# Kernel tuning notes

Hardware: AMD Instinct MI355X
Metric: run time of the kernel (lower is better)

## Reference

```python
import jax, jax.numpy as jnp
import numpy as np

B, F, DIM = 32, 2048, 1024
H, DH, Q, DEPTH, MULT = 16, 64, 64, 6, 2
INNER = H * DH  # 1024
EPS = 1e-5


def _ln(x, g, b):
    m = jnp.mean(x, axis=-1, keepdims=True)
    v = jnp.mean((x - m) ** 2, axis=-1, keepdims=True)
    return (x - m) / jnp.sqrt(v + EPS) * g + b


def setup_inputs() -> dict:
    key = jax.random.key(0)
    ks = iter(jax.random.split(key, 32))
    def rn(shape, s=0.02):
        return jax.random.normal(next(ks), shape, dtype=jnp.float32) * s
    inp = {
        "features": jax.random.normal(next(ks), (B, F, DIM), dtype=jnp.float32),
        "mask": jax.random.randint(next(ks), (B, F), 0, 2),
        "latents": jax.random.normal(next(ks), (Q, INNER), dtype=jnp.float32),
        "W_down": rn((DIM, INNER)),
        "nin_g": jnp.ones((DIM,)), "nin_b": jnp.zeros((DIM,)),
        "lf_g": jnp.ones((DEPTH, INNER)), "lf_b": jnp.zeros((DEPTH, INNER)),
        "ll_g": jnp.ones((DEPTH, INNER)), "ll_b": jnp.zeros((DEPTH, INNER)),
        "Wq": rn((DEPTH, INNER, INNER)),
        "Wk": rn((DEPTH, INNER, INNER)),
        "Wv": rn((DEPTH, INNER, INNER)),
        "ffln_g": jnp.ones((DEPTH, INNER)), "ffln_b": jnp.zeros((DEPTH, INNER)),
        "ff_w1": rn((DEPTH, INNER, MULT * INNER)),
        "ff_w2": rn((DEPTH, MULT * INNER, INNER)),
        "nout_g": jnp.ones((INNER,)), "nout_b": jnp.zeros((INNER,)),
    }
    return inp


def reference(features, mask, latents, W_down, nin_g, nin_b, lf_g, lf_b, ll_g, ll_b,
              Wq, Wk, Wv, ffln_g, ffln_b, ff_w1, ff_w2, nout_g, nout_b):
    scale = DH ** (-0.5)
    # input norm + projection down to inner_dim
    f = _ln(features, nin_g, nin_b) @ W_down            # (B, F, INNER)
    x = jnp.broadcast_to(latents, (B, Q, INNER))        # (B, Q, INNER)
    keep = (mask != 0)[:, None, None, :]                # (B, 1, 1, F)
    for i in range(DEPTH):
        xf = _ln(f, lf_g[i], lf_b[i])
        xl = _ln(x, ll_g[i], ll_b[i])
        q = (xl @ Wq[i]).reshape(B, Q, H, DH).transpose(0, 2, 1, 3) * scale  # bhqd
        k = (xf @ Wk[i]).reshape(B, F, H, DH).transpose(0, 2, 1, 3)          # bhfd
        v = (xf @ Wv[i]).reshape(B, F, H, DH).transpose(0, 2, 1, 3)          # bhfd
        sim = jnp.einsum('bhqd,bhfd->bhqf', q, k)
        sim = sim - jax.lax.stop_gradient(jnp.max(sim, axis=-1, keepdims=True))
        sim = jnp.where(keep, sim, -jnp.inf)
        alphas = jax.nn.softmax(sim, axis=-1)
        alphas = jnp.nan_to_num(alphas, nan=0.0)        # fully-masked rows -> 0
        out = jnp.einsum('bhqf,bhfd->bqhd', alphas, v).reshape(B, Q, INNER)
        # feed-forward: LN -> Linear -> ReLU -> Linear
        h = jax.nn.relu(_ln(out, ffln_g[i], ffln_b[i]) @ ff_w1[i]) @ ff_w2[i]
        x = x + h
    return _ln(x, nout_g, nout_b)
```

## Files before the change

### kernel.cpp

```cpp
#include <hip/hip_runtime.h>
#include <stdint.h>


#define DEV static __device__ __forceinline__

typedef __attribute__((ext_vector_type(8))) short short8;
typedef __attribute__((ext_vector_type(4))) float f32x4;
typedef __attribute__((ext_vector_type(4))) int int4v;
typedef __attribute__((ext_vector_type(4))) unsigned short ushort4v;
typedef unsigned short ushort_t;

DEV float bf2f(ushort_t u){ union{uint32_t i; float f;} x; x.i = ((uint32_t)u)<<16; return x.f; }
DEV ushort_t f2bf(float f){
  union{float f; uint32_t i;} x; x.f = f;
  uint32_t r = x.i + 0x7fffu + ((x.i>>16)&1u);
  return (ushort_t)(r>>16);
}

#define GLOAD16(gp, lp) __builtin_amdgcn_global_load_lds( \
    (const __attribute__((address_space(1))) uint32_t*)(gp), \
    (__attribute__((address_space(3))) uint32_t*)(lp), 16, 0, 0)

#define VMCNT(n) asm volatile("s_waitcnt vmcnt(" #n ")" ::: "memory")
#define CFENCE   asm volatile("" ::: "memory")
#define MFMA16(a,b,c) __builtin_amdgcn_mfma_f32_16x16x32_bf16(a,b,c,0,0,0)
#define MFMAI8(a,b,c) __builtin_amdgcn_mfma_i32_16x16x64_i8(a,b,c,0,0,0)

template<int NXB>
DEV void xcd_remapN(int g, int total, int& x, int& y){
  int xcd = g & 7;
  int k = g >> 3;
  int rows_per_xcd = (total / NXB) >> 3;
  y = xcd * rows_per_xcd + (k / NXB);
  x = k % NXB;
}

DEV void wreduce2(float& a, float& b){
  #pragma unroll
  for (int d = 32; d; d >>= 1){ a += __shfl_xor(a, d); b += __shfl_xor(b, d); }
}

__global__ __launch_bounds__(256) void k_compact(const int* __restrict__ mask,
                                                 int* __restrict__ idx, int* __restrict__ cnt){
  int b = blockIdx.x, t = threadIdx.x;
  const int* mb = mask + b*2048;
  int keep[8]; int c = 0;
  #pragma unroll
  for (int u = 0; u < 8; ++u){ keep[u] = (mb[t*8+u] != 0); c += keep[u]; }
  __shared__ int s[256];
  s[t] = c; __syncthreads();
  for (int off = 1; off < 256; off <<= 1){
    int v = (t >= off) ? s[t-off] : 0;
    __syncthreads();
    s[t] += v;
    __syncthreads();
  }
  int pos = s[t] - c;
  #pragma unroll
  for (int u = 0; u < 8; ++u) if (keep[u]) idx[b*2048 + pos++] = t*8 + u;
  if (t == 255) cnt[b] = s[255];
}

__global__ __launch_bounds__(256) void k_gather_norm(const float* __restrict__ feat,
        const int* __restrict__ idx, const int* __restrict__ cnt, ushort_t* __restrict__ outp){
  int w = threadIdx.x >> 6, l = threadIdx.x & 63;
  int row = blockIdx.x*4 + w;
  int b = row >> 11, j = row & 2047;
  if (j >= cnt[b]) return;
  int src = idx[b*2048 + j];
  const float* rp = feat + ((size_t)(b*2048 + src))*1024;
  float4 v[4]; float s = 0.f, q = 0.f;
  #pragma unroll
  for (int i = 0; i < 4; ++i){
    v[i] = *(const float4*)(rp + i*256 + l*4);
    s += v[i].x+v[i].y+v[i].z+v[i].w;
    q += v[i].x*v[i].x+v[i].y*v[i].y+v[i].z*v[i].z+v[i].w*v[i].w;
  }
  wreduce2(s, q);
  float mean = s * (1.f/1024.f);
  float rstd = rsqrtf(q*(1.f/1024.f) - mean*mean + 1e-5f);
  ushort_t* op = outp + (size_t)row*1024;
  #pragma unroll
  for (int i = 0; i < 4; ++i){
    ushort4v o;
    o.x = f2bf((v[i].x-mean)*rstd); o.y = f2bf((v[i].y-mean)*rstd);
    o.z = f2bf((v[i].z-mean)*rstd); o.w = f2bf((v[i].w-mean)*rstd);
    *(ushort4v*)(op + i*256 + l*4) = o;
  }
}

__global__ __launch_bounds__(256) void k_rownorm_i8(const ushort_t* __restrict__ in,
        int8_t* __restrict__ outp, float* __restrict__ sca, const int* __restrict__ cnt){
  int w = threadIdx.x >> 6, l = threadIdx.x & 63;
  int row = blockIdx.x*4 + w;
  if (cnt){ int b = row >> 11; if ((row & 2047) >= cnt[b]) return; }
  const ushort_t* rp = in + (size_t)row*1024 + l*16;
  float f[16]; float s = 0.f, q = 0.f;
  #pragma unroll
  for (int i = 0; i < 4; ++i){
    ushort4v u = *(const ushort4v*)(rp + i*4);
    f[i*4+0] = bf2f(u.x); f[i*4+1] = bf2f(u.y);
    f[i*4+2] = bf2f(u.z); f[i*4+3] = bf2f(u.w);
  }
  #pragma unroll
  for (int jj = 0; jj < 16; ++jj){ s += f[jj]; q += f[jj]*f[jj]; }
  wreduce2(s, q);
  float mean = s * (1.f/1024.f);
  float rstd = rsqrtf(q*(1.f/1024.f) - mean*mean + 1e-5f);
  float amax = 0.f;
  #pragma unroll
  for (int jj = 0; jj < 16; ++jj) amax = fmaxf(amax, fabsf(f[jj]-mean));
  #pragma unroll
  for (int d = 32; d; d >>= 1) amax = fmaxf(amax, __shfl_xor(amax, d));
  amax *= rstd;
  float inv = (amax > 0.f) ? 127.f/amax : 0.f;
  if (l == 0) sca[row] = amax * (1.f/127.f);
  uint32_t wds[4];
  #pragma unroll
  for (int i = 0; i < 4; ++i){
    uint32_t wd = 0;
    #pragma unroll
    for (int c = 0; c < 4; ++c){
      int qv = (int)rintf((f[i*4+c]-mean)*rstd*inv);
      wd |= ((uint32_t)(uint8_t)(int8_t)qv) << (c*8);
    }
    wds[i] = wd;
  }
  int4v pk; pk[0]=(int)wds[0]; pk[1]=(int)wds[1]; pk[2]=(int)wds[2]; pk[3]=(int)wds[3];
  *(int4v*)(outp + (size_t)row*1024 + l*16) = pk;
}

__global__ __launch_bounds__(256) void k_rownorm_f32_i8(const float* __restrict__ in,
        int8_t* __restrict__ outp, float* __restrict__ sca){
  int w = threadIdx.x >> 6, l = threadIdx.x & 63;
  int row = blockIdx.x*4 + w;
  const float* rp = in + (size_t)row*1024 + l*16;
  float f[16]; float s = 0.f, q = 0.f;
  #pragma unroll
  for (int i = 0; i < 4; ++i){
    float4 v = *(const float4*)(rp + i*4);
    f[i*4+0] = v.x; f[i*4+1] = v.y; f[i*4+2] = v.z; f[i*4+3] = v.w;
  }
  #pragma unroll
  for (int jj = 0; jj < 16; ++jj){ s += f[jj]; q += f[jj]*f[jj]; }
  wreduce2(s, q);
  float mean = s * (1.f/1024.f);
  float rstd = rsqrtf(q*(1.f/1024.f) - mean*mean + 1e-5f);
  float amax = 0.f;
  #pragma unroll
  for (int jj = 0; jj < 16; ++jj) amax = fmaxf(amax, fabsf(f[jj]-mean));
  #pragma unroll
  for (int d = 32; d; d >>= 1) amax = fmaxf(amax, __shfl_xor(amax, d));
  amax *= rstd;
  float inv = (amax > 0.f) ? 127.f/amax : 0.f;
  if (l == 0) sca[row] = amax * (1.f/127.f);
  uint32_t wds[4];
  #pragma unroll
  for (int i = 0; i < 4; ++i){
    uint32_t wd = 0;
    #pragma unroll
    for (int c = 0; c < 4; ++c){
      int qv = (int)rintf((f[i*4+c]-mean)*rstd*inv);
      wd |= ((uint32_t)(uint8_t)(int8_t)qv) << (c*8);
    }
    wds[i] = wd;
  }
  int4v pk; pk[0]=(int)wds[0]; pk[1]=(int)wds[1]; pk[2]=(int)wds[2]; pk[3]=(int)wds[3];
  *(int4v*)(outp + (size_t)row*1024 + l*16) = pk;
}

template<int PER>
__global__ __launch_bounds__(256) void k_quant_rows(const ushort_t* __restrict__ in,
        int8_t* __restrict__ outp, float* __restrict__ sca){
  const int K = PER*64;
  int w = threadIdx.x >> 6, l = threadIdx.x & 63;
  int row = blockIdx.x*4 + w;
  const ushort_t* rp = in + (size_t)row*K + l*PER;
  float f[PER];
  #pragma unroll
  for (int i = 0; i < PER/4; ++i){
    ushort4v u = *(const ushort4v*)(rp + i*4);
    f[i*4+0] = bf2f(u.x); f[i*4+1] = bf2f(u.y);
    f[i*4+2] = bf2f(u.z); f[i*4+3] = bf2f(u.w);
  }
  float amax = 0.f;
  #pragma unroll
  for (int jj = 0; jj < PER; ++jj) amax = fmaxf(amax, fabsf(f[jj]));
  #pragma unroll
  for (int d = 32; d; d >>= 1) amax = fmaxf(amax, __shfl_xor(amax, d));
  float inv = (amax > 0.f) ? 127.f/amax : 0.f;
  if (l == 0) sca[row] = amax * (1.f/127.f);
  #pragma unroll
  for (int vq = 0; vq < PER/16; ++vq){
    int4v pk;
    #pragma unroll
    for (int i = 0; i < 4; ++i){
      uint32_t wd = 0;
      #pragma unroll
      for (int c = 0; c < 4; ++c){
        int qv = (int)rintf(f[vq*16 + i*4 + c]*inv);
        wd |= ((uint32_t)(uint8_t)(int8_t)qv) << (c*8);
      }
      pk[i] = (int)wd;
    }
    *(int4v*)(outp + (size_t)row*K + l*PER + vq*16) = pk;
  }
}

__global__ __launch_bounds__(256) void k_final_ln(const float* __restrict__ x,
        const float* __restrict__ g, const float* __restrict__ bb, float* __restrict__ outp){
  int w = threadIdx.x >> 6, l = threadIdx.x & 63;
  int row = blockIdx.x*4 + w;
  const float* rp = x + (size_t)row*1024;
  float4 v[4]; float s = 0.f, q = 0.f;
  #pragma unroll
  for (int i = 0; i < 4; ++i){
    v[i] = *(const float4*)(rp + i*256 + l*4);
    s += v[i].x+v[i].y+v[i].z+v[i].w;
    q += v[i].x*v[i].x+v[i].y*v[i].y+v[i].z*v[i].z+v[i].w*v[i].w;
  }
  wreduce2(s, q);
  float mean = s * (1.f/1024.f);
  float rstd = rsqrtf(q*(1.f/1024.f) - mean*mean + 1e-5f);
  float* op = outp + (size_t)row*1024;
  #pragma unroll
  for (int i = 0; i < 4; ++i){
    float4 gg = *(const float4*)(g + i*256 + l*4);
    float4 bv = *(const float4*)(bb + i*256 + l*4);
    float4 o;
    o.x = (v[i].x-mean)*rstd*gg.x + bv.x; o.y = (v[i].y-mean)*rstd*gg.y + bv.y;
    o.z = (v[i].z-mean)*rstd*gg.z + bv.z; o.w = (v[i].w-mean)*rstd*gg.w + bv.w;
    *(float4*)(op + i*256 + l*4) = o;
  }
}

__global__ __launch_bounds__(256) void k_init_x(const float* __restrict__ lat, float* __restrict__ x){
  int v = blockIdx.x*256 + threadIdx.x;
  int row = v >> 8, cv = v & 255;
  ((float4*)x)[v] = ((const float4*)lat)[(row & 63)*256 + cv];
}

DEV void foldT_body(const float* __restrict__ W, const float* __restrict__ g,
                    float scale, ushort_t* __restrict__ Wt, int K, int N,
                    int n0, int k0){
  __shared__ float Ts[64][65];
  int t = threadIdx.x;
  #pragma unroll
  for (int i = 0; i < 4; ++i){
    int flat = i*1024 + t*4; int r = flat >> 6, c = flat & 63;
    float4 v = *(const float4*)(W + (size_t)(k0+r)*N + n0 + c);
    float gg = (g ? g[k0+r] : 1.f) * scale;
    Ts[r][c] = v.x*gg; Ts[r][c+1] = v.y*gg; Ts[r][c+2] = v.z*gg; Ts[r][c+3] = v.w*gg;
  }
  __syncthreads();
  #pragma unroll
  for (int i = 0; i < 4; ++i){
    int flat = i*1024 + t*4; int rn = flat >> 6, ck = flat & 63;
    ushort4v o;
    o.x = f2bf(Ts[ck][rn]);   o.y = f2bf(Ts[ck+1][rn]);
    o.z = f2bf(Ts[ck+2][rn]); o.w = f2bf(Ts[ck+3][rn]);
    *(ushort4v*)(Wt + (size_t)(n0+rn)*K + k0 + ck) = o;
  }
}

struct FDesc { const float* W; const float* g; ushort_t* dst; float scale; int K; int N; };
#define MAXFD 32
struct FoldTArgs { int cnt; FDesc d[MAXFD]; };

__global__ __launch_bounds__(256) void k_foldT_all(FoldTArgs a){
  const FDesc d = a.d[blockIdx.y];
  int nxb = d.N >> 6;
  int n0 = (blockIdx.x % nxb) * 64;
  int k0 = (blockIdx.x / nxb) * 64;
  if (k0 >= d.K) return;
  foldT_body(d.W, d.g, d.scale, d.dst, d.K, d.N, n0, k0);
}

DEV void foldBias_body(const float* __restrict__ W, const float* __restrict__ bvec,
                       float scale, float* __restrict__ bias, int K, int N, int o0){
  int t = threadIdx.x;
  int ol = t & 31, kc = t >> 5;
  int o = o0 + ol;
  int chunk = K >> 3;
  int c0 = kc*chunk, c1 = c0 + chunk;
  float s0 = 0, s1 = 0, s2 = 0, s3 = 0;
  for (int c = c0; c < c1; c += 4){
    s0 += bvec[c+0]*W[(size_t)(c+0)*N + o];
    s1 += bvec[c+1]*W[(size_t)(c+1)*N + o];
    s2 += bvec[c+2]*W[(size_t)(c+2)*N + o];
    s3 += bvec[c+3]*W[(size_t)(c+3)*N + o];
  }
  __shared__ float red[8][32];
  red[kc][ol] = (s0+s1)+(s2+s3);
  __syncthreads();
  if (kc == 0){
    float tot = 0;
    #pragma unroll
    for (int jj = 0; jj < 8; ++jj) tot += red[jj][ol];
    bias[o] = tot * scale;
  }
}

struct BDesc { const float* W; const float* b; float* dst; float scale; int K; int N; };
#define MAXBD 25
struct BiasArgs { int cnt; BDesc d[MAXBD]; };

__global__ __launch_bounds__(256) void k_foldBias_all(BiasArgs a){
  const BDesc d = a.d[blockIdx.y];
  int o0 = blockIdx.x * 32;
  if (o0 >= d.N) return;
  foldBias_body(d.W, d.b, d.scale, d.dst, d.K, d.N, o0);
}

template<int OUTMODE, int BN>
__global__ __launch_bounds__(256, 4) void k_gemm_sm(const int8_t* __restrict__ A,
        const int8_t* __restrict__ Bt, const float* __restrict__ sAr,
        const float* __restrict__ sBr, const float* __restrict__ bias,
        void* __restrict__ Cp, int M, int N, int Kb){
  constexpr int BM = 64;
  constexpr int NIF = BN/32;
  const int n0 = blockIdx.x * BN;
  const int m0 = blockIdx.y * BM;
  __shared__ __align__(16) char sA[2][BM*64];
  __shared__ __align__(16) char sB[2][BN*64];
  const int tid = threadIdx.x;
  const int wave = tid >> 6, lane = tid & 63;
  const int lo = lane & 15, hi = lane >> 4;
  const int wr = wave >> 1, wc = wave & 1;

  auto stage = [&](int buf, int k0){
    {
      int r = tid >> 2;
      int c = (tid & 3) ^ (r & 3);
      const int8_t* gp = A + (size_t)(m0 + r)*Kb + k0 + c*16;
      GLOAD16(gp, &sA[buf][0] + tid*16);
    }
    #pragma unroll
    for (int p = 0; p < BN/64; ++p){
      int r = p*64 + (tid >> 2);
      int c = (tid & 3) ^ (r & 3);
      const int8_t* gp = Bt + (size_t)(n0 + r)*Kb + k0 + c*16;
      GLOAD16(gp, &sB[buf][0] + p*4096 + tid*16);
    }
  };

  int4v acc[2][NIF] = {};
  stage(0, 0);
  const int nk = Kb >> 6;
  for (int ks = 0; ks < nk; ++ks){
    __syncthreads();
    if (ks + 1 < nk) stage((ks+1)&1, (ks+1) << 6);
    const int buf = ks & 1;
    int4v af[2], bfr[NIF];
    #pragma unroll
    for (int mi = 0; mi < 2; ++mi){
      int row = wr*(BM/2) + mi*16 + lo;
      af[mi] = *(const int4v*)(&sA[buf][row*64 + ((hi ^ (row & 3))*16)]);
    }
    #pragma unroll
    for (int ni = 0; ni < NIF; ++ni){
      int row = wc*(BN/2) + ni*16 + lo;
      bfr[ni] = *(const int4v*)(&sB[buf][row*64 + ((hi ^ (row & 3))*16)]);
    }
    #pragma unroll
    for (int mi = 0; mi < 2; ++mi)
      #pragma unroll
      for (int ni = 0; ni < NIF; ++ni)
        acc[mi][ni] = MFMAI8(af[mi], bfr[ni], acc[mi][ni]);
  }
  #pragma unroll
  for (int ni = 0; ni < NIF; ++ni){
    int col = n0 + wc*(BN/2) + ni*16 + lo;
    float bv = bias ? bias[col] : 0.f;
    float sb = sBr[col];
    #pragma unroll
    for (int mi = 0; mi < 2; ++mi){
      int rbase = m0 + wr*(BM/2) + mi*16 + hi*4;
      #pragma unroll
      for (int rr = 0; rr < 4; ++rr){
        int row = rbase + rr;
        float v = (float)acc[mi][ni][rr] * (sAr[row]*sb) + bv;
        size_t off = (size_t)row*N + col;
        if (OUTMODE == 0)      ((ushort_t*)Cp)[off] = f2bf(v);
        else if (OUTMODE == 1) ((ushort_t*)Cp)[off] = f2bf(fmaxf(v, 0.f));
        else                   ((float*)Cp)[off] += v;
      }
    }
  }
}

template<bool SKIP, int NXB>
__global__ __launch_bounds__(512, 2) void k_gemm256p8(const ushort_t* __restrict__ A,
        const ushort_t* __restrict__ Bt, const float* __restrict__ bias,
        ushort_t* __restrict__ Cp, int M, int N, int K, const int* __restrict__ cnt){
  int bx, by;
  xcd_remapN<NXB>(blockIdx.x, gridDim.x, bx, by);
  const int n0 = bx * 256;
  const int m0 = by * 256;
  if (SKIP){ int b = m0 >> 11; if ((m0 & 2047) >= cnt[b]) return; }
  __shared__ __align__(16) ushort_t sA[2][256*64];
  __shared__ __align__(16) ushort_t sB[2][256*64];
  const int tid = threadIdx.x;
  const int wave = tid >> 6, lane = tid & 63;
  const int lo = lane & 15, hi = lane >> 4;
  const int wm = wave >> 2, wn = wave & 3;
  const int srow = lane >> 3;
  const int schunk = (lane & 7) ^ srow;
  auto stageHalf = [&](ushort_t* dst, const ushort_t* __restrict__ G, int grow0,
                       int half, int k0){
    #pragma unroll
    for (int p = 0; p < 2; ++p){
      int rbase = half*128 + p*64 + wave*8;
      const ushort_t* gp = G + (size_t)(grow0 + rbase + srow)*K + k0 + schunk*8;
      char* lp = (char*)dst + (size_t)rbase*128;
      GLOAD16(gp, lp);
    }
  };
  auto ldsA = [&](int buf, int row, int kk)->short8{
    int ch = ((kk<<2) + hi) ^ (row & 7);
    return *(const short8*)((const char*)sA + (size_t)buf*32768 + (size_t)row*128 + ch*16);
  };
  auto ldsB = [&](int buf, int row, int kk)->short8{
    int ch = ((kk<<2) + hi) ^ (row & 7);
    return *(const short8*)((const char*)sB + (size_t)buf*32768 + (size_t)row*128 + ch*16);
  };
  f32x4 acc[8][4] = {};

  short8 af[4][2], bg[2][2];
#define LOADA(BUF, AH) \
    _Pragma("unroll") for (int mi_ = 0; mi_ < 4; ++mi_) \
      _Pragma("unroll") for (int kk_ = 0; kk_ < 2; ++kk_) \
        af[mi_][kk_] = ldsA(BUF, (AH)*128 + wm*64 + mi_*16 + lo, kk_);
#define LOADB(BUF, BH) \
    _Pragma("unroll") for (int nj_ = 0; nj_ < 2; ++nj_) \
      _Pragma("unroll") for (int kk_ = 0; kk_ < 2; ++kk_) \
        bg[nj_][kk_] = ldsB(BUF, (BH)*128 + wn*32 + nj_*16 + lo, kk_);
#define MMQ(AH, BH) \
    __builtin_amdgcn_s_barrier(); CFENCE; \
    __builtin_amdgcn_s_setprio(1); \
    _Pragma("unroll") for (int mi_ = 0; mi_ < 4; ++mi_) \
      _Pragma("unroll") for (int nj_ = 0; nj_ < 2; ++nj_) \
        _Pragma("unroll") for (int kk_ = 0; kk_ < 2; ++kk_) \
          acc[(AH)*4+mi_][(BH)*2+nj_] = \
            MFMA16(af[mi_][kk_], bg[nj_][kk_], acc[(AH)*4+mi_][(BH)*2+nj_]); \
    __builtin_amdgcn_s_setprio(0); CFENCE; \
    __builtin_amdgcn_s_barrier(); CFENCE;

  stageHalf(&sA[0][0], A,  m0, 0, 0);
  stageHalf(&sB[0][0], Bt, n0, 0, 0);
  stageHalf(&sA[0][0], A,  m0, 1, 0);
  stageHalf(&sB[0][0], Bt, n0, 1, 0);
  stageHalf(&sA[1][0], A,  m0, 0, 64);
  stageHalf(&sB[1][0], Bt, n0, 1, 64);
  VMCNT(4);
  __builtin_amdgcn_s_barrier();
  CFENCE;

  const int NI = K >> 7;
  for (int i = 0; i < NI; ++i){
    const int kt = i << 7;
    const bool lastI = (i == NI-1);
    LOADA(0,0) LOADB(0,0)
    stageHalf(&sA[1][0], A,  m0, 1, kt+64);
    MMQ(0,0)
    LOADB(0,1)
    stageHalf(&sB[1][0], Bt, n0, 0, kt+64);
    MMQ(0,1)
    LOADA(0,1)
    if (!lastI) stageHalf(&sA[0][0], A,  m0, 0, kt+128);
    MMQ(1,1)
    LOADB(0,0)
    if (!lastI) stageHalf(&sB[0][0], Bt, n0, 1, kt+128);
    if (lastI){ VMCNT(0); } else { VMCNT(4); }
    MMQ(1,0)
    LOADA(1,0) LOADB(1,0)
    if (!lastI) stageHalf(&sA[0][0], A,  m0, 1, kt+128);
    MMQ(0,0)
    LOADB(1,1)
    if (!lastI) stageHalf(&sB[0][0], Bt, n0, 0, kt+128);
    MMQ(0,1)
    LOADA(1,1)
    if (!lastI) stageHalf(&sA[1][0], A,  m0, 0, kt+192);
    MMQ(1,1)
    LOADB(1,0)
    if (!lastI){ stageHalf(&sB[1][0], Bt, n0, 1, kt+192); VMCNT(4); }
    MMQ(1,0)
  }
#undef LOADA
#undef LOADB
#undef MMQ

  #pragma unroll
  for (int b2 = 0; b2 < 2; ++b2)
    #pragma unroll
    for (int nj = 0; nj < 2; ++nj){
      int col = n0 + b2*128 + wn*32 + nj*16 + lo;
      float bv = bias ? bias[col] : 0.f;
      #pragma unroll
      for (int a2 = 0; a2 < 2; ++a2)
        #pragma unroll
        for (int mi4 = 0; mi4 < 4; ++mi4){
          int rbase = m0 + a2*128 + wm*64 + mi4*16 + hi*4;
          #pragma unroll
          for (int rr = 0; rr < 4; ++rr){
            float v = acc[a2*4+mi4][b2*2+nj][rr] + bv;
            Cp[(size_t)(rbase + rr)*N + col] = f2bf(v);
          }
        }
    }
}

template<bool SKIP, int NXB>
__global__ __launch_bounds__(512, 2) void k_gemm256i8(const int8_t* __restrict__ A,
        const int8_t* __restrict__ Bt, const float* __restrict__ sAr,
        const float* __restrict__ sBr, const float* __restrict__ bias,
        ushort_t* __restrict__ Cp, int M, int N, int Kb, const int* __restrict__ cnt){
  int bx, by;
  xcd_remapN<NXB>(blockIdx.x, gridDim.x, bx, by);
  const int n0 = bx * 256;
  const int m0 = by * 256;
  if (SKIP){ int b = m0 >> 11; if ((m0 & 2047) >= cnt[b]) return; }
  __shared__ __align__(16) char sAl[2][256*128];
  __shared__ __align__(16) char sBl[2][256*128];
  const int tid = threadIdx.x;
  const int wave = tid >> 6, lane = tid & 63;
  const int lo = lane & 15, hi = lane >> 4;
  const int wm = wave >> 2, wn = wave & 3;
  const int srow = lane >> 3;
  const int schunk = (lane & 7) ^ srow;
  auto stageHalf = [&](char* dst, const int8_t* __restrict__ G, int grow0,
                       int half, int k0){
    #pragma unroll
    for (int p = 0; p < 2; ++p){
      int rbase = half*128 + p*64 + wave*8;
      const int8_t* gp = G + (size_t)(grow0 + rbase + srow)*Kb + k0 + schunk*16;
      char* lp = dst + (size_t)rbase*128;
      GLOAD16(gp, lp);
    }
  };
  auto ldsA = [&](int buf, int row, int kk)->int4v{
    int ch = ((kk<<2) + hi) ^ (row & 7);
    return *(const int4v*)((const char*)sAl + (size_t)buf*32768 + (size_t)row*128 + ch*16);
  };
  auto ldsB = [&](int buf, int row, int kk)->int4v{
    int ch = ((kk<<2) + hi) ^ (row & 7);
    return *(const int4v*)((const char*)sBl + (size_t)buf*32768 + (size_t)row*128 + ch*16);
  };
  int4v acc[8][4] = {};

  int4v af[4][2], bg[2][2];
#define LOADA(BUF, AH) \
    _Pragma("unroll") for (int mi_ = 0; mi_ < 4; ++mi_) \
      _Pragma("unroll") for (int kk_ = 0; kk_ < 2; ++kk_) \
        af[mi_][kk_] = ldsA(BUF, (AH)*128 + wm*64 + mi_*16 + lo, kk_);
#define LOADB(BUF, BH) \
    _Pragma("unroll") for (int nj_ = 0; nj_ < 2; ++nj_) \
      _Pragma("unroll") for (int kk_ = 0; kk_ < 2; ++kk_) \
        bg[nj_][kk_] = ldsB(BUF, (BH)*128 + wn*32 + nj_*16 + lo, kk_);
#define MMQ(AH, BH) \
    __builtin_amdgcn_s_barrier(); CFENCE; \
    __builtin_amdgcn_s_setprio(1); \
    _Pragma("unroll") for (int mi_ = 0; mi_ < 4; ++mi_) \
      _Pragma("unroll") for (int nj_ = 0; nj_ < 2; ++nj_) \
        _Pragma("unroll") for (int kk_ = 0; kk_ < 2; ++kk_) \
          acc[(AH)*4+mi_][(BH)*2+nj_] = \
            MFMAI8(af[mi_][kk_], bg[nj_][kk_], acc[(AH)*4+mi_][(BH)*2+nj_]); \
    __builtin_amdgcn_s_setprio(0); CFENCE; \
    __builtin_amdgcn_s_barrier(); CFENCE;

  stageHalf(&sAl[0][0], A,  m0, 0, 0);
  stageHalf(&sBl[0][0], Bt, n0, 0, 0);
  stageHalf(&sAl[0][0], A,  m0, 1, 0);
  stageHalf(&sBl[0][0], Bt, n0, 1, 0);
  stageHalf(&sAl[1][0], A,  m0, 0, 128);
  stageHalf(&sBl[1][0], Bt, n0, 1, 128);
  VMCNT(4);
  __builtin_amdgcn_s_barrier();
  CFENCE;

  const int NI = Kb >> 8;
  for (int i = 0; i < NI; ++i){
    const int kt = i << 8;
    const bool lastI = (i == NI-1);
    LOADA(0,0) LOADB(0,0)
    stageHalf(&sAl[1][0], A,  m0, 1, kt+128);
    MMQ(0,0)
    LOADB(0,1)
    stageHalf(&sBl[1][0], Bt, n0, 0, kt+128);
    MMQ(0,1)
    LOADA(0,1)
    if (!lastI) stageHalf(&sAl[0][0], A,  m0, 0, kt+256);
    MMQ(1,1)
    LOADB(0,0)
    if (!lastI) stageHalf(&sBl[0][0], Bt, n0, 1, kt+256);
    if (lastI){ VMCNT(0); } else { VMCNT(4); }
    MMQ(1,0)
    LOADA(1,0) LOADB(1,0)
    if (!lastI) stageHalf(&sAl[0][0], A,  m0, 1, kt+256);
    MMQ(0,0)
    LOADB(1,1)
    if (!lastI) stageHalf(&sBl[0][0], Bt, n0, 0, kt+256);
    MMQ(0,1)
    LOADA(1,1)
    if (!lastI) stageHalf(&sAl[1][0], A,  m0, 0, kt+384);
    MMQ(1,1)
    LOADB(1,0)
    if (!lastI){ stageHalf(&sBl[1][0], Bt, n0, 1, kt+384); VMCNT(4); }
    MMQ(1,0)
  }
#undef LOADA
#undef LOADB
#undef MMQ

  #pragma unroll
  for (int b2 = 0; b2 < 2; ++b2)
    #pragma unroll
    for (int nj = 0; nj < 2; ++nj){
      int col = n0 + b2*128 + wn*32 + nj*16 + lo;
      float bv = bias ? bias[col] : 0.f;
      float sb = sBr[col];
      #pragma unroll
      for (int a2 = 0; a2 < 2; ++a2)
        #pragma unroll
        for (int mi4 = 0; mi4 < 4; ++mi4){
          int rbase = m0 + a2*128 + wm*64 + mi4*16 + hi*4;
          #pragma unroll
          for (int rr = 0; rr < 4; ++rr){
            int row = rbase + rr;
            float v = (float)acc[a2*4+mi4][b2*2+nj][rr] * (sAr[row]*sb) + bv;
            Cp[(size_t)row*N + col] = f2bf(v);
          }
        }
    }
}

__global__ __launch_bounds__(256) void k_attn(const ushort_t* __restrict__ qb,
        const ushort_t* __restrict__ kvb, int kstride, const int* __restrict__ cnt,
        ushort_t* __restrict__ outb){
  const int bh = blockIdx.x;
  const int b = bh >> 4, h = bh & 15;
  const int t = threadIdx.x;
  const int wave = t >> 6, lane = t & 63, lo = lane & 15, hi = lane >> 4;
  __shared__ ushort_t Qs[64*64];
  __shared__ ushort_t Ks[2][64*64];
  __shared__ ushort_t Vt[2][64][72];
  __shared__ ushort_t Ps[4][16][72];

  const int count = cnt[b];

  #pragma unroll
  for (int p = 0; p < 2; ++p){
    int r = p*32 + wave*8 + (lane >> 3);
    int c = (lane & 7) ^ (r & 7);
    const ushort_t* gp = qb + (size_t)(b*64 + r)*1024 + h*64 + c*8;
    char* lp = (char*)Qs + p*4096 + wave*1024;
    GLOAD16(gp, lp);
  }

  auto stageK = [&](int buf, int tt){
    #pragma unroll
    for (int p = 0; p < 2; ++p){
      int r = p*32 + wave*8 + (lane >> 3);
      int c = (lane & 7) ^ (r & 7);
      const ushort_t* gp = kvb + (size_t)(b*2048 + tt*64 + r)*kstride + h*64 + c*8;
      char* lp = (char*)(&Ks[buf][0]) + p*4096 + wave*1024;
      GLOAD16(gp, lp);
    }
  };
  const int vjj = (t & 31)*2, vc = (t >> 5)*8;
  ushort4v va0, va1, vb0, vb1;
  auto issueV = [&](int tt){
    const ushort_t* g0 = kvb + (size_t)(b*2048 + tt*64 + vjj)*kstride + 1024 + h*64 + vc;
    va0 = *(const ushort4v*)(g0);
    va1 = *(const ushort4v*)(g0 + 4);
    vb0 = *(const ushort4v*)(g0 + kstride);
    vb1 = *(const ushort4v*)(g0 + kstride + 4);
  };
  auto writeV = [&](int buf, int tt){
    bool va  = (tt*64 + vjj)     < count;
    bool vb2 = (tt*64 + vjj + 1) < count;
    #pragma unroll
    for (int u = 0; u < 8; ++u){
      ushort_t ea = (u < 4) ? ((ushort_t*)&va0)[u] : ((ushort_t*)&va1)[u-4];
      ushort_t eb = (u < 4) ? ((ushort_t*)&vb0)[u] : ((ushort_t*)&vb1)[u-4];
      uint32_t word = (va ? (uint32_t)ea : 0u) | ((vb2 ? (uint32_t)eb : 0u) << 16);
      *(uint32_t*)(&Vt[buf][vc+u][vjj]) = word;
    }
  };

  f32x4 oacc[4] = {};
  float m[4], l[4];
  #pragma unroll
  for (int rr = 0; rr < 4; ++rr){ m[rr] = -__builtin_inff(); l[rr] = 0.f; }

  const int ntiles = (count + 63) >> 6;
  if (ntiles > 0){ stageK(0, 0); issueV(0); }

  for (int tt = 0; tt < ntiles; ++tt){
    const int buf = tt & 1;
    writeV(buf, tt);
    if (tt + 1 < ntiles){ stageK(buf^1, tt+1); issueV(tt+1); }
    asm volatile("s_waitcnt lgkmcnt(0)" ::: "memory");
    __builtin_amdgcn_s_barrier();
    CFENCE;

    f32x4 s[4] = {};
    #pragma unroll
    for (int kk = 0; kk < 2; ++kk){
      int rA = wave*16 + lo;
      short8 aq = *(const short8*)(&Qs[rA*64 + (((kk*4 + hi) ^ (rA & 7))*8)]);
      #pragma unroll
      for (int ni = 0; ni < 4; ++ni){
        int rB = ni*16 + lo;
        short8 bk = *(const short8*)(&Ks[buf][rB*64 + (((kk*4 + hi) ^ (rB & 7))*8)]);
        s[ni] = MFMA16(aq, bk, s[ni]);
      }
    }
    #pragma unroll
    for (int ni = 0; ni < 4; ++ni){
      if (tt*64 + ni*16 + lo >= count){
        s[ni][0] = s[ni][1] = s[ni][2] = s[ni][3] = -__builtin_inff();
      }
    }
    float p[4][4];
    #pragma unroll
    for (int rr = 0; rr < 4; ++rr){
      float mx = fmaxf(fmaxf(s[0][rr], s[1][rr]), fmaxf(s[2][rr], s[3][rr]));
      #pragma unroll
      for (int d = 1; d < 16; d <<= 1) mx = fmaxf(mx, __shfl_xor(mx, d));
      float mnew = fmaxf(m[rr], mx);
      float sc = __expf(m[rr] - mnew);
      float rsum = 0.f;
      #pragma unroll
      for (int ni = 0; ni < 4; ++ni){
        float pv = __expf(s[ni][rr] - mnew);
        p[ni][rr] = pv;
        rsum += pv;
      }
      #pragma unroll
      for (int d = 1; d < 16; d <<= 1) rsum += __shfl_xor(rsum, d);
      l[rr] = l[rr]*sc + rsum;
      m[rr] = mnew;
      #pragma unroll
      for (int ni = 0; ni < 4; ++ni) oacc[ni][rr] *= sc;
    }
    #pragma unroll
    for (int ni = 0; ni < 4; ++ni)
      #pragma unroll
      for (int rr = 0; rr < 4; ++rr)
        Ps[wave][hi*4+rr][ni*16+lo] = f2bf(p[ni][rr]);
    asm volatile("s_waitcnt lgkmcnt(0)" ::: "memory");
    #pragma unroll
    for (int kk = 0; kk < 2; ++kk){
      short8 pa = *(const short8*)(&Ps[wave][lo][kk*32 + hi*8]);
      #pragma unroll
      for (int ni = 0; ni < 4; ++ni){
        short8 bv = *(const short8*)(&Vt[buf][ni*16 + lo][kk*32 + hi*8]);
        oacc[ni] = MFMA16(pa, bv, oacc[ni]);
      }
    }
    CFENCE;
    __builtin_amdgcn_s_barrier();
    CFENCE;
  }
  #pragma unroll
  for (int rr = 0; rr < 4; ++rr){
    float inv = (l[rr] > 0.f) ? 1.f/l[rr] : 0.f;
    #pragma unroll
    for (int ni = 0; ni < 4; ++ni){
      size_t off = (size_t)(b*64 + wave*16 + hi*4 + rr)*1024 + h*64 + ni*16 + lo;
      outb[off] = f2bf(oacc[ni][rr] * inv);
    }
  }
}

extern "C" void kernel_launch(void* const* d_in, const int* in_sizes, int n_in,
                              void* d_out, int out_size, void* d_ws, size_t ws_size,
                              hipStream_t stream){
  const float* features = (const float*)d_in[0];
  const int*   mask     = (const int*)  d_in[1];
  const float* latents  = (const float*)d_in[2];
  const float* W_down   = (const float*)d_in[3];
  const float* nin_g    = (const float*)d_in[4];
  const float* nin_b    = (const float*)d_in[5];
  const float* lf_g     = (const float*)d_in[6];
  const float* lf_b     = (const float*)d_in[7];
  const float* ll_g     = (const float*)d_in[8];
  const float* ll_b     = (const float*)d_in[9];
  const float* Wq       = (const float*)d_in[10];
  const float* Wk       = (const float*)d_in[11];
  const float* Wv       = (const float*)d_in[12];
  const float* ffln_g   = (const float*)d_in[13];
  const float* ffln_b   = (const float*)d_in[14];
  const float* ff_w1    = (const float*)d_in[15];
  const float* ff_w2    = (const float*)d_in[16];
  const float* nout_g   = (const float*)d_in[17];
  const float* nout_b   = (const float*)d_in[18];

  char* ws = (char*)d_ws;
  size_t off = 0;
  auto alloc = [&](size_t bytes)->char*{
    char* p = ws + off;
    off += (bytes + 255) & ~(size_t)255;
    return p;
  };
  const size_t SZW = (size_t)1024*1024*2;

  ushort_t* FHAT  = (ushort_t*)alloc((size_t)65536*1024*2);
  int8_t*   I8A   = (int8_t*)  alloc((size_t)65536*1024);
  float*    SA    = (float*)   alloc((size_t)65536*4);
  int8_t*   I8KV  = (int8_t*)  alloc((size_t)12288*1024);
  float*    SKV   = (float*)   alloc((size_t)12288*4);
  int8_t*   I8Q   = (int8_t*)  alloc((size_t)6144*1024);
  float*    SQW   = (float*)   alloc((size_t)6144*4);
  int8_t*   I8W1  = (int8_t*)  alloc((size_t)12288*1024);
  float*    SW1   = (float*)   alloc((size_t)12288*4);
  int8_t*   I8W2  = (int8_t*)  alloc((size_t)6144*2048);
  float*    SW2   = (float*)   alloc((size_t)6144*4);
  ushort_t* WDT   = (ushort_t*)alloc(SZW);
  ushort_t* WQT6  = (ushort_t*)alloc(SZW*6);
  ushort_t* WKVT6 = (ushort_t*)alloc(SZW*2*6);
  ushort_t* W1T6  = (ushort_t*)alloc(SZW*2*6);
  ushort_t* W2T6  = (ushort_t*)alloc(SZW*2*6);
  float* BD   = (float*)alloc(1024*4);
  float* BQ6  = (float*)alloc(1024*4*6);
  float* BKV6 = (float*)alloc(2048*4*6);
  float* B16  = (float*)alloc(2048*4*6);
  float*    X    = (float*)   alloc((size_t)2048*1024*4);
  int8_t*   I8X  = (int8_t*)  alloc((size_t)2048*1024);
  float*    SX   = (float*)   alloc((size_t)2048*4);
  ushort_t* QP   = (ushort_t*)alloc((size_t)2048*1024*2);
  ushort_t* OUTB = (ushort_t*)alloc((size_t)2048*1024*2);
  int8_t*   I8O  = (int8_t*)  alloc((size_t)2048*1024);
  float*    SO   = (float*)   alloc((size_t)2048*4);
  ushort_t* H1   = (ushort_t*)alloc((size_t)2048*2048*2);
  int8_t*   I8H  = (int8_t*)  alloc((size_t)2048*2048);
  float*    SH   = (float*)   alloc((size_t)2048*4);
  int* CNT = (int*)alloc(32*4);
  int* IDX = (int*)alloc((size_t)65536*4);
  ushort_t* KVBUF = (ushort_t*)alloc((size_t)65536*2048*2);
  ushort_t* FNORM = KVBUF;
  (void)in_sizes; (void)n_in; (void)out_size; (void)ws_size;

  const float scale = 0.125f;

  FoldTArgs fa; int nf = 0;
  auto addF = [&](const float* W, const float* g, float sc, ushort_t* dst, int K, int N){
    fa.d[nf++] = FDesc{W, g, dst, sc, K, N};
  };
  addF(W_down, nin_g, 1.f, WDT, 1024, 1024);
  for (int i = 0; i < 6; ++i){
    const float* Wqi = Wq + (size_t)i*1024*1024;
    const float* Wki = Wk + (size_t)i*1024*1024;
    const float* Wvi = Wv + (size_t)i*1024*1024;
    const float* W1i = ff_w1 + (size_t)i*1024*2048;
    const float* W2i = ff_w2 + (size_t)i*2048*1024;
    addF(Wqi, ll_g + i*1024, scale, WQT6  + i*(SZW/2),        1024, 1024);
    addF(Wki, lf_g + i*1024, 1.f,   WKVT6 + i*SZW,            1024, 1024);
    addF(Wvi, lf_g + i*1024, 1.f,   WKVT6 + i*SZW + (SZW/2),  1024, 1024);
    addF(W1i, ffln_g + i*1024, 1.f, W1T6  + i*SZW,            1024, 2048);
    addF(W2i, nullptr, 1.f,         W2T6  + i*SZW,            2048, 1024);
  }
  fa.cnt = nf;

  BiasArgs ba; int nb = 0;
  auto addB = [&](const float* W, const float* b, float sc, float* dst, int K, int N){
    ba.d[nb++] = BDesc{W, b, dst, sc, K, N};
  };
  addB(W_down, nin_b, 1.f, BD, 1024, 1024);
  for (int i = 0; i < 6; ++i){
    const float* Wqi = Wq + (size_t)i*1024*1024;
    const float* Wki = Wk + (size_t)i*1024*1024;
    const float* Wvi = Wv + (size_t)i*1024*1024;
    const float* W1i = ff_w1 + (size_t)i*1024*2048;
    addB(Wqi, ll_b + i*1024, scale, BQ6  + i*1024,        1024, 1024);
    addB(Wki, lf_b + i*1024, 1.f,   BKV6 + i*2048,        1024, 1024);
    addB(Wvi, lf_b + i*1024, 1.f,   BKV6 + i*2048 + 1024, 1024, 1024);
    addB(W1i, ffln_b + i*1024, 1.f, B16  + i*2048,        1024, 2048);
  }
  ba.cnt = nb;

  k_compact     <<<32,    256, 0, stream>>>(mask, IDX, CNT);
  k_gather_norm <<<16384, 256, 0, stream>>>(features, IDX, CNT, FNORM);
  k_foldT_all   <<<dim3(512, nf), 256, 0, stream>>>(fa);
  k_foldBias_all<<<dim3(64,  nb), 256, 0, stream>>>(ba);
  k_quant_rows<16><<<3072, 256, 0, stream>>>(WKVT6, I8KV, SKV);
  k_quant_rows<16><<<1536, 256, 0, stream>>>(WQT6,  I8Q,  SQW);
  k_quant_rows<16><<<3072, 256, 0, stream>>>(W1T6,  I8W1, SW1);
  k_quant_rows<32><<<1536, 256, 0, stream>>>(W2T6,  I8W2, SW2);
  k_gemm256p8<true,4><<<1024, 512, 0, stream>>>(FNORM, WDT, BD, FHAT, 65536, 1024, 1024, CNT);
  k_rownorm_i8  <<<16384, 256, 0, stream>>>(FHAT, I8A, SA, CNT);
  k_init_x      <<<2048,  256, 0, stream>>>(latents, X);

  for (int i = 0; i < 6; ++i){
    k_gemm256i8<true,8><<<2048, 512, 0, stream>>>(I8A, I8KV + (size_t)i*2048*1024,
                                                  SA, SKV + i*2048, BKV6 + i*2048,
                                                  KVBUF, 65536, 2048, 1024, CNT);
    k_rownorm_f32_i8<<<512, 256, 0, stream>>>(X, I8X, SX);
    k_gemm_sm<0,64><<<dim3(16,32), 256, 0, stream>>>(I8X, I8Q + (size_t)i*1024*1024,
                                                     SX, SQW + i*1024, BQ6 + i*1024,
                                                     QP, 2048, 1024, 1024);
    k_attn<<<512, 256, 0, stream>>>(QP, KVBUF, 2048, CNT, OUTB);
    k_rownorm_i8<<<512, 256, 0, stream>>>(OUTB, I8O, SO, nullptr);
    k_gemm_sm<1,128><<<dim3(16,32), 256, 0, stream>>>(I8O, I8W1 + (size_t)i*2048*1024,
                                                      SO, SW1 + i*2048, B16 + i*2048,
                                                      H1, 2048, 2048, 1024);
    k_quant_rows<32><<<512, 256, 0, stream>>>(H1, I8H, SH);
    k_gemm_sm<2,64><<<dim3(16,32), 256, 0, stream>>>(I8H, I8W2 + (size_t)i*1024*2048,
                                                     SH, SW2 + i*1024, nullptr,
                                                     X, 2048, 1024, 2048);
  }
  k_final_ln<<<512, 256, 0, stream>>>(X, nout_g, nout_b, (float*)d_out);
}
```

Measured before the change: 1.640 ms.

## Split attention over key halves and batch K/V projection across layer pairs

Attention is split into two key-range halves per (batch, head), writing fp32 partial outputs plus row max and sum, and a new combine kernel merges them into bf16. The K/V projection GEMM now runs every other layer with N=4096, producing K/V for two consecutive layers at once into a doubled buffer. The split raises attention parallelism, and the batched GEMM reduces launches and improves GEMM efficiency. The cost is extra fp32 partial traffic, an extra kernel, and a larger workspace.

Result: slower. 2.036 ms (+24.1%).

```diff
diff --git a/kernel.cpp b/kernel.cpp
--- a/kernel.cpp
+++ b/kernel.cpp
@@ -634,10 +634,11 @@
     }
 }
 
-__global__ __launch_bounds__(256) void k_attn(const ushort_t* __restrict__ qb,
+__global__ __launch_bounds__(256) void k_attn_split(const ushort_t* __restrict__ qb,
         const ushort_t* __restrict__ kvb, int kstride, const int* __restrict__ cnt,
-        ushort_t* __restrict__ outb){
-  const int bh = blockIdx.x;
+        float* __restrict__ PO, float* __restrict__ PM, float* __restrict__ PL){
+  const int c = blockIdx.x & 1;
+  const int bh = blockIdx.x >> 1;
   const int b = bh >> 4, h = bh & 15;
   const int t = threadIdx.x;
   const int wave = t >> 6, lane = t & 63, lo = lane & 15, hi = lane >> 4;
@@ -647,12 +648,15 @@
   __shared__ ushort_t Ps[4][16][72];
 
   const int count = cnt[b];
+  const int kbase = c * 1024;
+  int rem = count - kbase;
+  const int ntiles = (rem > 0) ? ((rem + 63) >> 6 < 16 ? (rem + 63) >> 6 : 16) : 0;
 
   #pragma unroll
   for (int p = 0; p < 2; ++p){
     int r = p*32 + wave*8 + (lane >> 3);
-    int c = (lane & 7) ^ (r & 7);
-    const ushort_t* gp = qb + (size_t)(b*64 + r)*1024 + h*64 + c*8;
+    int cc = (lane & 7) ^ (r & 7);
+    const ushort_t* gp = qb + (size_t)(b*64 + r)*1024 + h*64 + cc*8;
     char* lp = (char*)Qs + p*4096 + wave*1024;
     GLOAD16(gp, lp);
   }
@@ -661,8 +665,8 @@
     #pragma unroll
     for (int p = 0; p < 2; ++p){
       int r = p*32 + wave*8 + (lane >> 3);
-      int c = (lane & 7) ^ (r & 7);
-      const ushort_t* gp = kvb + (size_t)(b*2048 + tt*64 + r)*kstride + h*64 + c*8;
+      int cc = (lane & 7) ^ (r & 7);
+      const ushort_t* gp = kvb + (size_t)(b*2048 + kbase + tt*64 + r)*kstride + h*64 + cc*8;
       char* lp = (char*)(&Ks[buf][0]) + p*4096 + wave*1024;
       GLOAD16(gp, lp);
     }
@@ -670,15 +674,15 @@
   const int vjj = (t & 31)*2, vc = (t >> 5)*8;
   ushort4v va0, va1, vb0, vb1;
   auto issueV = [&](int tt){
-    const ushort_t* g0 = kvb + (size_t)(b*2048 + tt*64 + vjj)*kstride + 1024 + h*64 + vc;
+    const ushort_t* g0 = kvb + (size_t)(b*2048 + kbase + tt*64 + vjj)*kstride + 1024 + h*64 + vc;
     va0 = *(const ushort4v*)(g0);
     va1 = *(const ushort4v*)(g0 + 4);
     vb0 = *(const ushort4v*)(g0 + kstride);
     vb1 = *(const ushort4v*)(g0 + kstride + 4);
   };
   auto writeV = [&](int buf, int tt){
-    bool va  = (tt*64 + vjj)     < count;
-    bool vb2 = (tt*64 + vjj + 1) < count;
+    bool va  = (kbase + tt*64 + vjj)     < count;
+    bool vb2 = (kbase + tt*64 + vjj + 1) < count;
     #pragma unroll
     for (int u = 0; u < 8; ++u){
       ushort_t ea = (u < 4) ? ((ushort_t*)&va0)[u] : ((ushort_t*)&va1)[u-4];
@@ -693,7 +697,6 @@
   #pragma unroll
   for (int rr = 0; rr < 4; ++rr){ m[rr] = -__builtin_inff(); l[rr] = 0.f; }
 
-  const int ntiles = (count + 63) >> 6;
   if (ntiles > 0){ stageK(0, 0); issueV(0); }
 
   for (int tt = 0; tt < ntiles; ++tt){
@@ -718,7 +721,7 @@
     }
     #pragma unroll
     for (int ni = 0; ni < 4; ++ni){
-      if (tt*64 + ni*16 + lo >= count){
+      if (kbase + tt*64 + ni*16 + lo >= count){
         s[ni][0] = s[ni][1] = s[ni][2] = s[ni][3] = -__builtin_inff();
       }
     }
@@ -765,12 +768,44 @@
   }
   #pragma unroll
   for (int rr = 0; rr < 4; ++rr){
-    float inv = (l[rr] > 0.f) ? 1.f/l[rr] : 0.f;
+    int row = b*64 + wave*16 + hi*4 + rr;
+    if (lo == 0){
+      PM[(size_t)(c*2048 + row)*16 + h] = m[rr];
+      PL[(size_t)(c*2048 + row)*16 + h] = l[rr];
+    }
     #pragma unroll
     for (int ni = 0; ni < 4; ++ni){
-      size_t off = (size_t)(b*64 + wave*16 + hi*4 + rr)*1024 + h*64 + ni*16 + lo;
-      outb[off] = f2bf(oacc[ni][rr] * inv);
-    }
+      PO[(size_t)(c*2048 + row)*1024 + h*64 + ni*16 + lo] = oacc[ni][rr];
+    }
+  }
+}
+
+__global__ __launch_bounds__(256) void k_combine(const float* __restrict__ PO,
+        const float* __restrict__ PM, const float* __restrict__ PL,
+        ushort_t* __restrict__ outb){
+  int w = threadIdx.x >> 6, l = threadIdx.x & 63;
+  int row = blockIdx.x*4 + w;
+  int h = l >> 2, d0 = (l & 3)*16;
+  float m0 = PM[(size_t)row*16 + h],        l0 = PL[(size_t)row*16 + h];
+  float m1 = PM[(size_t)(2048 + row)*16 + h], l1 = PL[(size_t)(2048 + row)*16 + h];
+  float M = fmaxf(m0, m1);
+  float e0 = (l0 > 0.f) ? __expf(m0 - M) : 0.f;
+  float e1 = (l1 > 0.f) ? __expf(m1 - M) : 0.f;
+  float L = l0*e0 + l1*e1;
+  float inv = (L > 0.f) ? 1.f/L : 0.f;
+  const float* p0 = PO + (size_t)row*1024 + h*64 + d0;
+  const float* p1 = PO + (size_t)(2048 + row)*1024 + h*64 + d0;
+  ushort_t* op = outb + (size_t)row*1024 + h*64 + d0;
+  #pragma unroll
+  for (int i = 0; i < 4; ++i){
+    float4 a = *(const float4*)(p0 + i*4);
+    float4 bq = *(const float4*)(p1 + i*4);
+    ushort4v o;
+    o.x = f2bf((a.x*e0 + bq.x*e1)*inv);
+    o.y = f2bf((a.y*e0 + bq.y*e1)*inv);
+    o.z = f2bf((a.z*e0 + bq.z*e1)*inv);
+    o.w = f2bf((a.w*e0 + bq.w*e1)*inv);
+    *(ushort4v*)(op + i*4) = o;
   }
 }
 
@@ -836,9 +871,12 @@
   ushort_t* H1   = (ushort_t*)alloc((size_t)2048*2048*2);
   int8_t*   I8H  = (int8_t*)  alloc((size_t)2048*2048);
   float*    SH   = (float*)   alloc((size_t)2048*4);
+  float*    PO   = (float*)   alloc((size_t)2*2048*1024*4);
+  float*    PM   = (float*)   alloc((size_t)2*2048*16*4);
+  float*    PL   = (float*)   alloc((size_t)2*2048*16*4);
   int* CNT = (int*)alloc(32*4);
   int* IDX = (int*)alloc((size_t)65536*4);
-  ushort_t* KVBUF = (ushort_t*)alloc((size_t)65536*2048*2);
+  ushort_t* KVBUF = (ushort_t*)alloc((size_t)65536*4096*2);
   ushort_t* FNORM = KVBUF;
   (void)in_sizes; (void)n_in; (void)out_size; (void)ws_size;
 
@@ -893,14 +931,18 @@
   k_init_x      <<<2048,  256, 0, stream>>>(latents, X);
 
   for (int i = 0; i < 6; ++i){
-    k_gemm256i8<true,8><<<2048, 512, 0, stream>>>(I8A, I8KV + (size_t)i*2048*1024,
-                                                  SA, SKV + i*2048, BKV6 + i*2048,
-                                                  KVBUF, 65536, 2048, 1024, CNT);
+    if ((i & 1) == 0){
+      k_gemm256i8<true,16><<<4096, 512, 0, stream>>>(I8A, I8KV + (size_t)i*2048*1024,
+                                                     SA, SKV + i*2048, BKV6 + i*2048,
+                                                     KVBUF, 65536, 4096, 1024, CNT);
+    }
     k_rownorm_f32_i8<<<512, 256, 0, stream>>>(X, I8X, SX);
     k_gemm_sm<0,64><<<dim3(16,32), 256, 0, stream>>>(I8X, I8Q + (size_t)i*1024*1024,
                                                      SX, SQW + i*1024, BQ6 + i*1024,
                                                      QP, 2048, 1024, 1024);
-    k_attn<<<512, 256, 0, stream>>>(QP, KVBUF, 2048, CNT, OUTB);
+    k_attn_split<<<1024, 256, 0, stream>>>(QP, KVBUF + (size_t)(i & 1)*2048, 4096,
+                                           CNT, PO, PM, PL);
+    k_combine<<<512, 256, 0, stream>>>(PO, PM, PL, OUTB);
     k_rownorm_i8<<<512, 256, 0, stream>>>(OUTB, I8O, SO, nullptr);
     k_gemm_sm<1,128><<<dim3(16,32), 256, 0, stream>>>(I8O, I8W1 + (size_t)i*2048*1024,
                                                       SO, SW1 + i*2048, B16 + i*2048,
```
